# Performance work log

Hardware: AMD Instinct MI355X
Metric: run time of the kernel (lower is better)

The kernel has to match this reference:

```python
import jax, jax.numpy as jnp
import numpy as np

MAX_AGENTS = 64
IN_DIM = 256
HID_DIM = 512
OUT_DIM = 256
MAX_CHILDREN = 8
BATCH = 1024


def setup_inputs() -> dict:
    key = jax.random.key(0)
    k1, k2, k3, k4, k5 = jax.random.split(key, 5)
    W1 = jax.random.normal(k1, (MAX_AGENTS, IN_DIM, HID_DIM), dtype=jnp.float32) * 0.02
    b1 = jnp.zeros((MAX_AGENTS, HID_DIM), dtype=jnp.float32)
    W2 = jax.random.normal(k2, (MAX_AGENTS, HID_DIM, OUT_DIM), dtype=jnp.float32) * 0.02
    b2 = jnp.zeros((MAX_AGENTS, OUT_DIM), dtype=jnp.float32)
    router_weights = jax.random.normal(k3, (MAX_AGENTS, HID_DIM, MAX_CHILDREN), dtype=jnp.float32) * 0.01
    agent_indices = jax.random.randint(k4, (BATCH,), 0, MAX_AGENTS, dtype=jnp.int64 if jax.config.jax_enable_x64 else jnp.int32)
    x = jax.random.normal(k5, (BATCH, IN_DIM), dtype=jnp.float32)
    return {
        "x": x,
        "W1": W1,
        "b1": b1,
        "W2": W2,
        "b2": b2,
        "router_weights": router_weights,
        "agent_indices": agent_indices,
    }


def reference(x, W1, b1, W2, b2, router_weights, agent_indices):
    # Gather per-sample weights (same as torch advanced indexing W1[agent_indices])
    w1 = W1[agent_indices]           # [B, In, Hid]
    b1g = b1[agent_indices]          # [B, Hid]
    w2 = W2[agent_indices]           # [B, Hid, Out]
    b2g = b2[agent_indices]          # [B, Out]
    rw = router_weights[agent_indices]  # [B, Hid, C]

    # per-sample MLP: bmm with a singleton row -> einsum
    h = jax.nn.relu(jnp.einsum('bi,bih->bh', x, w1) + b1g)      # [B, Hid]
    out = jnp.einsum('bh,bho->bo', h, w2) + b2g                 # [B, Out]
    r_logits = jnp.einsum('bh,bhc->bc', h, rw)                  # [B, C]
    return (h, out, r_logits)
```

## Files before the change

kernel.cpp:

```cpp
#include <hip/hip_runtime.h>

#define IN_DIM   256
#define HID_DIM  512
#define OUT_DIM  256
#define N_CHILD  8
#define BATCH    1024

#define SB    16
#define XPAD  20
#define MAXCH 128

extern "C" __global__ __launch_bounds__(1024)
void prep_sort(const int* __restrict__ raw, int* __restrict__ sorted,
               int* __restrict__ ch_agent, int* __restrict__ ch_start,
               int* __restrict__ ch_len, float* __restrict__ zdst)
{
    const int t = threadIdx.x;
    if (blockIdx.x > 0) {
        const int total4 = (BATCH * (OUT_DIM + N_CHILD)) / 4;
        const float4 z = make_float4(0.f, 0.f, 0.f, 0.f);
        for (int i = (blockIdx.x - 1) * 1024 + t; i < total4; i += 4 * 1024)
            ((float4*)zdst)[i] = z;
        return;
    }
    __shared__ int cnt[64], cnt2[64], start[64];
    __shared__ int is32, totch;
    if (t < 64) { cnt[t] = 0; cnt2[t] = 0; }
    if (t == 0) is32 = 0;
    __syncthreads();
    if (raw[2 * (t & 511) + 1] != 0) is32 = 1;
    __syncthreads();
    const int a = (is32 ? raw[t] : raw[2 * t]) & 63;
    atomicAdd(&cnt[a], 1);
    __syncthreads();
    if (t < 64) {
        const int c   = cnt[t];
        const int nch = (c + SB - 1) / SB;
        int sc = c, sn = nch;
        #pragma unroll
        for (int d = 1; d < 64; d <<= 1) {
            const int vc = __shfl_up(sc, d);
            const int vn = __shfl_up(sn, d);
            if (t >= d) { sc += vc; sn += vn; }
        }
        const int off = sc - c;
        start[t] = off;
        const int chb = sn - nch;
        for (int p = 0, j = 0; p < c; p += SB, ++j) {
            ch_agent[chb + j] = t;
            ch_start[chb + j] = off + p;
            ch_len[chb + j]   = (c - p < SB) ? (c - p) : SB;
        }
        if (t == 63) totch = sn;
    }
    __syncthreads();
    if (t >= totch && t < MAXCH) ch_len[t] = 0;
    const int pos = start[a] + atomicAdd(&cnt2[a], 1);
    sorted[pos] = t;
}

extern "C" __global__ __launch_bounds__(256)
void k1_mlp1(const float* __restrict__ x, const float* __restrict__ W1,
             const float* __restrict__ b1, const float* __restrict__ rw,
             const int* __restrict__ sorted, const int* __restrict__ ch_agent,
             const int* __restrict__ ch_start, const int* __restrict__ ch_len,
             float* __restrict__ h_out, float* __restrict__ r_out)
{
    const int chunk = blockIdx.x;
    const int len = ch_len[chunk];
    if (len == 0) return;
    const int a  = ch_agent[chunk];
    const int cs = ch_start[chunk];
    const int t  = threadIdx.x;
    const int bcol = blockIdx.y * 64;

    __shared__ float xT[IN_DIM * XPAD];
    __shared__ float wS[64 * 64];
    __shared__ int   sid[SB];

    if (t < SB) sid[t] = sorted[cs + (t < len ? t : len - 1)];
    __syncthreads();

    #pragma unroll
    for (int s = 0; s < SB; ++s)
        xT[t * XPAD + s] = x[(size_t)sid[s] * IN_DIM + t];

    const float* Wb = W1 + (size_t)a * IN_DIM * HID_DIM + bcol;
    const int cg = t & 15;
    const int kq = (t >> 4) & 3;
    const int w  = t >> 6;
    const bool act = (w * 4) < len;

    float acc[16];
    #pragma unroll
    for (int i = 0; i < 16; ++i) acc[i] = 0.f;

    for (int p = 0; p < IN_DIM / 64; ++p) {
        __syncthreads();
        #pragma unroll
        for (int i = 0; i < 4; ++i) {
            const int id  = t + i * 256;
            const int row = id >> 4;
            const int c4  = (id & 15) * 4;
            *(float4*)(&wS[row * 64 + c4]) =
                *(const float4*)(Wb + (size_t)(p * 64 + row) * HID_DIM + c4);
        }
        __syncthreads();
        if (act) {
            #pragma unroll
            for (int i = 0; i < 16; ++i) {
                const int row = i * 4 + kq;
                const float4 wv = *(const float4*)(&wS[row * 64 + cg * 4]);
                const float4 xv = *(const float4*)(&xT[(p * 64 + row) * XPAD + w * 4]);
                const float wa[4] = {wv.x, wv.y, wv.z, wv.w};
                const float xa[4] = {xv.x, xv.y, xv.z, xv.w};
                #pragma unroll
                for (int c = 0; c < 4; ++c)
                    #pragma unroll
                    for (int s = 0; s < 4; ++s)
                        acc[c * 4 + s] = fmaf(wa[c], xa[s], acc[c * 4 + s]);
            }
        }
    }

    if (!act) return;

    #pragma unroll
    for (int i = 0; i < 16; ++i) {
        acc[i] += __shfl_xor(acc[i], 16);
        acc[i] += __shfl_xor(acc[i], 32);
    }

    if (kq != 0) return;

    const float4 bv = *(const float4*)(b1 + a * HID_DIM + bcol + cg * 4);
    const float ba[4] = {bv.x, bv.y, bv.z, bv.w};
    float hv[16];
    #pragma unroll
    for (int c = 0; c < 4; ++c)
        #pragma unroll
        for (int s = 0; s < 4; ++s)
            hv[c * 4 + s] = fmaxf(acc[c * 4 + s] + ba[c], 0.f);

    #pragma unroll
    for (int s = 0; s < 4; ++s) {
        float4 v = make_float4(hv[0 * 4 + s], hv[1 * 4 + s],
                               hv[2 * 4 + s], hv[3 * 4 + s]);
        *(float4*)(h_out + (size_t)sid[w * 4 + s] * HID_DIM + bcol + cg * 4) = v;
    }

    float rp[32];
    #pragma unroll
    for (int i = 0; i < 32; ++i) rp[i] = 0.f;
    const float* rwa = rw + (size_t)a * HID_DIM * N_CHILD
                          + (size_t)(bcol + cg * 4) * N_CHILD;
    #pragma unroll
    for (int j = 0; j < 4; ++j)
        #pragma unroll
        for (int ch = 0; ch < 8; ++ch) {
            const float rv = rwa[j * N_CHILD + ch];
            #pragma unroll
            for (int s = 0; s < 4; ++s)
                rp[s * 8 + ch] = fmaf(hv[j * 4 + s], rv, rp[s * 8 + ch]);
        }
    #pragma unroll
    for (int i = 0; i < 32; ++i) {
        rp[i] += __shfl_xor(rp[i], 1);
        rp[i] += __shfl_xor(rp[i], 2);
        rp[i] += __shfl_xor(rp[i], 4);
        rp[i] += __shfl_xor(rp[i], 8);
    }
    if (cg == 0) {
        #pragma unroll
        for (int s = 0; s < 4; ++s) {
            const int sg = w * 4 + s;
            if (sg < len) {
                float* rdst = r_out + (size_t)sid[sg] * N_CHILD;
                #pragma unroll
                for (int ch = 0; ch < 8; ++ch)
                    atomicAdd(rdst + ch, rp[s * 8 + ch]);
            }
        }
    }
}

extern "C" __global__ __launch_bounds__(256)
void k2_mlp2(const float* __restrict__ h, const float* __restrict__ W2,
             const float* __restrict__ b2,
             const int* __restrict__ sorted, const int* __restrict__ ch_agent,
             const int* __restrict__ ch_start, const int* __restrict__ ch_len,
             float* __restrict__ o_out)
{
    const int chunk = blockIdx.x;
    const int len = ch_len[chunk];
    if (len == 0) return;
    const int a  = ch_agent[chunk];
    const int cs = ch_start[chunk];
    const int t  = threadIdx.x;
    const int bcol = blockIdx.y * 64;
    const int kb   = blockIdx.z * 256;

    __shared__ float hT[64 * XPAD];
    __shared__ float wS[64 * 64];
    __shared__ int   sid[SB];

    if (t < SB) sid[t] = sorted[cs + (t < len ? t : len - 1)];
    __syncthreads();

    const float* Wb = W2 + (size_t)a * HID_DIM * OUT_DIM + bcol;
    const int cg = t & 15;
    const int kq = (t >> 4) & 3;
    const int w  = t >> 6;
    const bool act = (w * 4) < len;

    float acc[16];
    #pragma unroll
    for (int i = 0; i < 16; ++i) acc[i] = 0.f;

    for (int p = 0; p < 4; ++p) {
        const int k0 = kb + p * 64;
        __syncthreads();
        {
            const int row = t & 63;
            const int sb  = (t >> 6) * 4;
            #pragma unroll
            for (int j = 0; j < 4; ++j)
                hT[row * XPAD + sb + j] =
                    h[(size_t)sid[sb + j] * HID_DIM + k0 + row];
        }
        #pragma unroll
        for (int i = 0; i < 4; ++i) {
            const int id  = t + i * 256;
            const int r2  = id >> 4;
            const int c4  = (id & 15) * 4;
            *(float4*)(&wS[r2 * 64 + c4]) =
                *(const float4*)(Wb + (size_t)(k0 + r2) * OUT_DIM + c4);
        }
        __syncthreads();
        if (act) {
            #pragma unroll
            for (int i = 0; i < 16; ++i) {
                const int row = i * 4 + kq;
                const float4 wv = *(const float4*)(&wS[row * 64 + cg * 4]);
                const float4 xv = *(const float4*)(&hT[row * XPAD + w * 4]);
                const float wa[4] = {wv.x, wv.y, wv.z, wv.w};
                const float xa[4] = {xv.x, xv.y, xv.z, xv.w};
                #pragma unroll
                for (int c = 0; c < 4; ++c)
                    #pragma unroll
                    for (int s = 0; s < 4; ++s)
                        acc[c * 4 + s] = fmaf(wa[c], xa[s], acc[c * 4 + s]);
            }
        }
    }

    if (!act) return;
    #pragma unroll
    for (int i = 0; i < 16; ++i) {
        acc[i] += __shfl_xor(acc[i], 16);
        acc[i] += __shfl_xor(acc[i], 32);
    }
    if (kq == 0) {
        float4 bv = make_float4(0.f, 0.f, 0.f, 0.f);
        if (blockIdx.z == 0)
            bv = *(const float4*)(b2 + a * OUT_DIM + bcol + cg * 4);
        #pragma unroll
        for (int s = 0; s < 4; ++s) {
            const int g = w * 4 + s;
            if (g < len) {
                float* op = o_out + (size_t)sid[g] * OUT_DIM + bcol + cg * 4;
                atomicAdd(op + 0, acc[0 * 4 + s] + bv.x);
                atomicAdd(op + 1, acc[1 * 4 + s] + bv.y);
                atomicAdd(op + 2, acc[2 * 4 + s] + bv.z);
                atomicAdd(op + 3, acc[3 * 4 + s] + bv.w);
            }
        }
    }
}

extern "C" void kernel_launch(void* const* d_in, const int* in_sizes, int n_in,
                              void* d_out, int out_size, void* d_ws, size_t ws_size,
                              hipStream_t stream) {
    const float* x  = (const float*)d_in[0];
    const float* W1 = (const float*)d_in[1];
    const float* b1 = (const float*)d_in[2];
    const float* W2 = (const float*)d_in[3];
    const float* b2 = (const float*)d_in[4];
    const float* rw = (const float*)d_in[5];
    const int* raw  = (const int*)d_in[6];

    int* ws       = (int*)d_ws;
    int* sorted   = ws;
    int* ch_agent = ws + 1024;
    int* ch_start = ws + 1152;
    int* ch_len   = ws + 1280;

    float* out   = (float*)d_out;
    float* h_out = out;
    float* o_out = h_out + (size_t)BATCH * HID_DIM;
    float* r_out = o_out + (size_t)BATCH * OUT_DIM;

    hipLaunchKernelGGL(prep_sort, dim3(5), dim3(1024), 0, stream,
                       raw, sorted, ch_agent, ch_start, ch_len, o_out);
    hipLaunchKernelGGL(k1_mlp1, dim3(MAXCH, 8), dim3(256), 0, stream,
                       x, W1, b1, rw, sorted, ch_agent, ch_start, ch_len,
                       h_out, r_out);
    hipLaunchKernelGGL(k2_mlp2, dim3(MAXCH, 4, 2), dim3(256), 0, stream,
                       h_out, W2, b2, sorted, ch_agent, ch_start, ch_len, o_out);
}
```

Before: 132.6 us.

## Fuse both MLP layers into one kernel, splitting layer 2 over hidden slices

Merges the layer-1 and layer-2 kernels. Each block computes a 64-wide slice of h, keeps it in shared memory, and then multiplies it by the matching 64 rows of W2 across all 256 output columns, accumulating into the output with atomics. This removes one kernel launch and the global round-trip of h between layers. The W tile is halved to 32 rows with a min-blocks-per-CU launch bound of 4 to raise occupancy. In exchange, layer 2 is now split 8 ways over K instead of 2, so output atomics rise by about four times. The extra syncs for the smaller tiles may also serialize the work.

```diff
diff --git a/kernel.cpp b/kernel.cpp
--- a/kernel.cpp
+++ b/kernel.cpp
@@ -59,12 +59,14 @@
     sorted[pos] = t;
 }
 
-extern "C" __global__ __launch_bounds__(256)
-void k1_mlp1(const float* __restrict__ x, const float* __restrict__ W1,
-             const float* __restrict__ b1, const float* __restrict__ rw,
+extern "C" __global__ __launch_bounds__(256, 4)
+void k_fused(const float* __restrict__ x, const float* __restrict__ W1,
+             const float* __restrict__ b1, const float* __restrict__ W2,
+             const float* __restrict__ b2, const float* __restrict__ rw,
              const int* __restrict__ sorted, const int* __restrict__ ch_agent,
              const int* __restrict__ ch_start, const int* __restrict__ ch_len,
-             float* __restrict__ h_out, float* __restrict__ r_out)
+             float* __restrict__ h_out, float* __restrict__ o_out,
+             float* __restrict__ r_out)
 {
     const int chunk = blockIdx.x;
     const int len = ch_len[chunk];
@@ -75,7 +77,8 @@
     const int bcol = blockIdx.y * 64;
 
     __shared__ float xT[IN_DIM * XPAD];
-    __shared__ float wS[64 * 64];
+    __shared__ float hT[64 * XPAD];
+    __shared__ float wS[32 * 64];
     __shared__ int   sid[SB];
 
     if (t < SB) sid[t] = sorted[cs + (t < len ? t : len - 1)];
@@ -85,33 +88,33 @@
     for (int s = 0; s < SB; ++s)
         xT[t * XPAD + s] = x[(size_t)sid[s] * IN_DIM + t];
 
-    const float* Wb = W1 + (size_t)a * IN_DIM * HID_DIM + bcol;
     const int cg = t & 15;
     const int kq = (t >> 4) & 3;
     const int w  = t >> 6;
     const bool act = (w * 4) < len;
 
+    const float* Wb = W1 + (size_t)a * IN_DIM * HID_DIM + bcol;
     float acc[16];
     #pragma unroll
     for (int i = 0; i < 16; ++i) acc[i] = 0.f;
 
-    for (int p = 0; p < IN_DIM / 64; ++p) {
+    for (int p = 0; p < IN_DIM / 32; ++p) {
         __syncthreads();
         #pragma unroll
-        for (int i = 0; i < 4; ++i) {
+        for (int i = 0; i < 2; ++i) {
             const int id  = t + i * 256;
             const int row = id >> 4;
             const int c4  = (id & 15) * 4;
             *(float4*)(&wS[row * 64 + c4]) =
-                *(const float4*)(Wb + (size_t)(p * 64 + row) * HID_DIM + c4);
+                *(const float4*)(Wb + (size_t)(p * 32 + row) * HID_DIM + c4);
         }
         __syncthreads();
         if (act) {
             #pragma unroll
-            for (int i = 0; i < 16; ++i) {
+            for (int i = 0; i < 8; ++i) {
                 const int row = i * 4 + kq;
                 const float4 wv = *(const float4*)(&wS[row * 64 + cg * 4]);
-                const float4 xv = *(const float4*)(&xT[(p * 64 + row) * XPAD + w * 4]);
+                const float4 xv = *(const float4*)(&xT[(p * 32 + row) * XPAD + w * 4]);
                 const float wa[4] = {wv.x, wv.y, wv.z, wv.w};
                 const float xa[4] = {xv.x, xv.y, xv.z, xv.w};
                 #pragma unroll
@@ -123,156 +126,126 @@
         }
     }
 
-    if (!act) return;
-
     #pragma unroll
     for (int i = 0; i < 16; ++i) {
         acc[i] += __shfl_xor(acc[i], 16);
         acc[i] += __shfl_xor(acc[i], 32);
     }
 
-    if (kq != 0) return;
-
-    const float4 bv = *(const float4*)(b1 + a * HID_DIM + bcol + cg * 4);
-    const float ba[4] = {bv.x, bv.y, bv.z, bv.w};
-    float hv[16];
-    #pragma unroll
-    for (int c = 0; c < 4; ++c)
-        #pragma unroll
-        for (int s = 0; s < 4; ++s)
-            hv[c * 4 + s] = fmaxf(acc[c * 4 + s] + ba[c], 0.f);
-
-    #pragma unroll
-    for (int s = 0; s < 4; ++s) {
-        float4 v = make_float4(hv[0 * 4 + s], hv[1 * 4 + s],
-                               hv[2 * 4 + s], hv[3 * 4 + s]);
-        *(float4*)(h_out + (size_t)sid[w * 4 + s] * HID_DIM + bcol + cg * 4) = v;
-    }
-
-    float rp[32];
-    #pragma unroll
-    for (int i = 0; i < 32; ++i) rp[i] = 0.f;
-    const float* rwa = rw + (size_t)a * HID_DIM * N_CHILD
-                          + (size_t)(bcol + cg * 4) * N_CHILD;
-    #pragma unroll
-    for (int j = 0; j < 4; ++j)
-        #pragma unroll
-        for (int ch = 0; ch < 8; ++ch) {
-            const float rv = rwa[j * N_CHILD + ch];
+    if (act && kq == 0) {
+        const float4 bv = *(const float4*)(b1 + a * HID_DIM + bcol + cg * 4);
+        const float ba[4] = {bv.x, bv.y, bv.z, bv.w};
+        float hv[16];
+        #pragma unroll
+        for (int c = 0; c < 4; ++c)
             #pragma unroll
             for (int s = 0; s < 4; ++s)
-                rp[s * 8 + ch] = fmaf(hv[j * 4 + s], rv, rp[s * 8 + ch]);
-        }
-    #pragma unroll
-    for (int i = 0; i < 32; ++i) {
-        rp[i] += __shfl_xor(rp[i], 1);
-        rp[i] += __shfl_xor(rp[i], 2);
-        rp[i] += __shfl_xor(rp[i], 4);
-        rp[i] += __shfl_xor(rp[i], 8);
-    }
-    if (cg == 0) {
+                hv[c * 4 + s] = fmaxf(acc[c * 4 + s] + ba[c], 0.f);
+
         #pragma unroll
         for (int s = 0; s < 4; ++s) {
-            const int sg = w * 4 + s;
-            if (sg < len) {
-                float* rdst = r_out + (size_t)sid[sg] * N_CHILD;
-                #pragma unroll
-                for (int ch = 0; ch < 8; ++ch)
-                    atomicAdd(rdst + ch, rp[s * 8 + ch]);
-            }
-        }
-    }
-}
-
-extern "C" __global__ __launch_bounds__(256)
-void k2_mlp2(const float* __restrict__ h, const float* __restrict__ W2,
-             const float* __restrict__ b2,
-             const int* __restrict__ sorted, const int* __restrict__ ch_agent,
-             const int* __restrict__ ch_start, const int* __restrict__ ch_len,
-             float* __restrict__ o_out)
-{
-    const int chunk = blockIdx.x;
-    const int len = ch_len[chunk];
-    if (len == 0) return;
-    const int a  = ch_agent[chunk];
-    const int cs = ch_start[chunk];
-    const int t  = threadIdx.x;
-    const int bcol = blockIdx.y * 64;
-    const int kb   = blockIdx.z * 256;
-
-    __shared__ float hT[64 * XPAD];
-    __shared__ float wS[64 * 64];
-    __shared__ int   sid[SB];
-
-    if (t < SB) sid[t] = sorted[cs + (t < len ? t : len - 1)];
-    __syncthreads();
-
-    const float* Wb = W2 + (size_t)a * HID_DIM * OUT_DIM + bcol;
-    const int cg = t & 15;
-    const int kq = (t >> 4) & 3;
-    const int w  = t >> 6;
-    const bool act = (w * 4) < len;
-
-    float acc[16];
-    #pragma unroll
-    for (int i = 0; i < 16; ++i) acc[i] = 0.f;
-
-    for (int p = 0; p < 4; ++p) {
-        const int k0 = kb + p * 64;
-        __syncthreads();
-        {
-            const int row = t & 63;
-            const int sb  = (t >> 6) * 4;
-            #pragma unroll
-            for (int j = 0; j < 4; ++j)
-                hT[row * XPAD + sb + j] =
-                    h[(size_t)sid[sb + j] * HID_DIM + k0 + row];
-        }
-        #pragma unroll
-        for (int i = 0; i < 4; ++i) {
-            const int id  = t + i * 256;
-            const int r2  = id >> 4;
-            const int c4  = (id & 15) * 4;
-            *(float4*)(&wS[r2 * 64 + c4]) =
-                *(const float4*)(Wb + (size_t)(k0 + r2) * OUT_DIM + c4);
-        }
-        __syncthreads();
+            float4 v = make_float4(hv[0 * 4 + s], hv[1 * 4 + s],
+                                   hv[2 * 4 + s], hv[3 * 4 + s]);
+            *(float4*)(h_out + (size_t)sid[w * 4 + s] * HID_DIM + bcol + cg * 4) = v;
+        }
+        #pragma unroll
+        for (int c = 0; c < 4; ++c)
+            #pragma unroll
+            for (int s = 0; s < 4; ++s)
+                hT[(cg * 4 + c) * XPAD + (w * 4 + s)] = hv[c * 4 + s];
+
+        float rp[32];
+        #pragma unroll
+        for (int i = 0; i < 32; ++i) rp[i] = 0.f;
+        const float* rwa = rw + (size_t)a * HID_DIM * N_CHILD
+                              + (size_t)(bcol + cg * 4) * N_CHILD;
+        #pragma unroll
+        for (int j = 0; j < 4; ++j)
+            #pragma unroll
+            for (int ch = 0; ch < 8; ++ch) {
+                const float rv = rwa[j * N_CHILD + ch];
+                #pragma unroll
+                for (int s = 0; s < 4; ++s)
+                    rp[s * 8 + ch] = fmaf(hv[j * 4 + s], rv, rp[s * 8 + ch]);
+            }
+        #pragma unroll
+        for (int i = 0; i < 32; ++i) {
+            rp[i] += __shfl_xor(rp[i], 1);
+            rp[i] += __shfl_xor(rp[i], 2);
+            rp[i] += __shfl_xor(rp[i], 4);
+            rp[i] += __shfl_xor(rp[i], 8);
+        }
+        if (cg == 0) {
+            #pragma unroll
+            for (int s = 0; s < 4; ++s) {
+                const int sg = w * 4 + s;
+                if (sg < len) {
+                    float* rdst = r_out + (size_t)sid[sg] * N_CHILD;
+                    #pragma unroll
+                    for (int ch = 0; ch < 8; ++ch)
+                        atomicAdd(rdst + ch, rp[s * 8 + ch]);
+                }
+            }
+        }
+    }
+    __syncthreads();
+
+    const float* W2b = W2 + ((size_t)a * HID_DIM + bcol) * OUT_DIM;
+    for (int q = 0; q < 4; ++q) {
+        const int oc = q * 64;
+        float ac2[16];
+        #pragma unroll
+        for (int i = 0; i < 16; ++i) ac2[i] = 0.f;
+
+        for (int kp = 0; kp < 2; ++kp) {
+            __syncthreads();
+            #pragma unroll
+            for (int i = 0; i < 2; ++i) {
+                const int id  = t + i * 256;
+                const int row = id >> 4;
+                const int c4  = (id & 15) * 4;
+                *(float4*)(&wS[row * 64 + c4]) =
+                    *(const float4*)(W2b + (size_t)(kp * 32 + row) * OUT_DIM + oc + c4);
+            }
+            __syncthreads();
+            if (act) {
+                #pragma unroll
+                for (int i = 0; i < 8; ++i) {
+                    const int row = i * 4 + kq;
+                    const float4 wv = *(const float4*)(&wS[row * 64 + cg * 4]);
+                    const float4 xv = *(const float4*)(&hT[(kp * 32 + row) * XPAD + w * 4]);
+                    const float wa[4] = {wv.x, wv.y, wv.z, wv.w};
+                    const float xa[4] = {xv.x, xv.y, xv.z, xv.w};
+                    #pragma unroll
+                    for (int c = 0; c < 4; ++c)
+                        #pragma unroll
+                        for (int s = 0; s < 4; ++s)
+                            ac2[c * 4 + s] = fmaf(wa[c], xa[s], ac2[c * 4 + s]);
+                }
+            }
+        }
+
         if (act) {
             #pragma unroll
             for (int i = 0; i < 16; ++i) {
-                const int row = i * 4 + kq;
-                const float4 wv = *(const float4*)(&wS[row * 64 + cg * 4]);
-                const float4 xv = *(const float4*)(&hT[row * XPAD + w * 4]);
-                const float wa[4] = {wv.x, wv.y, wv.z, wv.w};
-                const float xa[4] = {xv.x, xv.y, xv.z, xv.w};
-                #pragma unroll
-                for (int c = 0; c < 4; ++c)
-                    #pragma unroll
-                    for (int s = 0; s < 4; ++s)
-                        acc[c * 4 + s] = fmaf(wa[c], xa[s], acc[c * 4 + s]);
-            }
-        }
-    }
-
-    if (!act) return;
-    #pragma unroll
-    for (int i = 0; i < 16; ++i) {
-        acc[i] += __shfl_xor(acc[i], 16);
-        acc[i] += __shfl_xor(acc[i], 32);
-    }
-    if (kq == 0) {
-        float4 bv = make_float4(0.f, 0.f, 0.f, 0.f);
-        if (blockIdx.z == 0)
-            bv = *(const float4*)(b2 + a * OUT_DIM + bcol + cg * 4);
-        #pragma unroll
-        for (int s = 0; s < 4; ++s) {
-            const int g = w * 4 + s;
-            if (g < len) {
-                float* op = o_out + (size_t)sid[g] * OUT_DIM + bcol + cg * 4;
-                atomicAdd(op + 0, acc[0 * 4 + s] + bv.x);
-                atomicAdd(op + 1, acc[1 * 4 + s] + bv.y);
-                atomicAdd(op + 2, acc[2 * 4 + s] + bv.z);
-                atomicAdd(op + 3, acc[3 * 4 + s] + bv.w);
+                ac2[i] += __shfl_xor(ac2[i], 16);
+                ac2[i] += __shfl_xor(ac2[i], 32);
+            }
+            if (kq == 0) {
+                float4 bv = make_float4(0.f, 0.f, 0.f, 0.f);
+                if (blockIdx.y == 0)
+                    bv = *(const float4*)(b2 + a * OUT_DIM + oc + cg * 4);
+                #pragma unroll
+                for (int s = 0; s < 4; ++s) {
+                    const int g = w * 4 + s;
+                    if (g < len) {
+                        float* op = o_out + (size_t)sid[g] * OUT_DIM + oc + cg * 4;
+                        atomicAdd(op + 0, ac2[0 * 4 + s] + bv.x);
+                        atomicAdd(op + 1, ac2[1 * 4 + s] + bv.y);
+                        atomicAdd(op + 2, ac2[2 * 4 + s] + bv.z);
+                        atomicAdd(op + 3, ac2[3 * 4 + s] + bv.w);
+                    }
+                }
             }
         }
     }
@@ -302,9 +275,8 @@
 
     hipLaunchKernelGGL(prep_sort, dim3(5), dim3(1024), 0, stream,
                        raw, sorted, ch_agent, ch_start, ch_len, o_out);
-    hipLaunchKernelGGL(k1_mlp1, dim3(MAXCH, 8), dim3(256), 0, stream,
-                       x, W1, b1, rw, sorted, ch_agent, ch_start, ch_len,
-                       h_out, r_out);
-    hipLaunchKernelGGL(k2_mlp2, dim3(MAXCH, 4, 2), dim3(256), 0, stream,
-                       h_out, W2, b2, sorted, ch_agent, ch_start, ch_len, o_out);
+    hipLaunchKernelGGL(k_fused, dim3(MAXCH, 8), dim3(256), 0, stream,
+                       x, W1, b1, W2, b2, rw,
+                       sorted, ch_agent, ch_start, ch_len,
+                       h_out, o_out, r_out);
 }
```

Result: slower. 148.1 us (+11.7%).
